# Kernel tuning notes

Hardware: AMD Instinct MI355X
Metric: run time of the kernel (lower is better)

Reference implementation:

```python
import jax, jax.numpy as jnp
import numpy as np
from itertools import combinations

UNSPOOL = np.array([h + b for h in combinations(range(0, 4), 2) for b in combinations(range(4, 9), 3)])  # (60,5)
EMB = 64

def _lrelu(v):
    return jax.nn.leaky_relu(v, 0.01)

def _unspool(x):
    # x: (M,18) int -> (1,M,60,5) ranks, suits
    x = x[None]
    ranks, suits = x[:, :, ::2], x[:, :, 1::2]
    hr, hs = ranks[:, :, :4], suits[:, :, :4]
    br, bs = ranks[:, :, 4:], suits[:, :, 4:]
    hi, bi = jnp.argsort(hs, -1), jnp.argsort(bs, -1)
    hr = jnp.take_along_axis(hr, hi, -1); hs = jnp.take_along_axis(hs, hi, -1)
    br = jnp.take_along_axis(br, bi, -1); bs = jnp.take_along_axis(bs, bi, -1)
    hi2, bi2 = jnp.argsort(hr, -1), jnp.argsort(br, -1)
    r = jnp.concatenate([jnp.take_along_axis(hr, hi2, -1), jnp.take_along_axis(br, bi2, -1)], -1)
    s = jnp.concatenate([jnp.take_along_axis(hs, hi2, -1), jnp.take_along_axis(bs, bi2, -1)], -1)
    return r[:, :, UNSPOOL], s[:, :, UNSPOOL]

def setup_inputs() -> dict:
    key = jax.random.key(0)
    ks = jax.random.split(key, 24)
    M, nA = 2048, 9
    ranks = jax.random.randint(ks[0], (M, 9), 1, 14)
    suits = jax.random.randint(ks[1], (M, 9), 1, 5)
    x = jnp.zeros((M, 18), jnp.int64 if jax.config.jax_enable_x64 else jnp.int32)
    x = x.at[:, ::2].set(ranks).at[:, 1::2].set(suits)
    def lin(k, i, o):
        kw, kb = jax.random.split(k)
        s = 1.0 / np.sqrt(i)
        return (jax.random.uniform(kw, (i, o), jnp.float32, -s, s),
                jax.random.uniform(kb, (o,), jnp.float32, -s, s))
    emb = jax.random.normal(ks[2], (53, EMB), jnp.float32)
    emb = emb.at[0].set(0.0)  # padding_idx=0
    hW1, hb1 = lin(ks[3], 128, 512); hW2, hb2 = lin(ks[4], 512, 128)
    bW1, bb1 = lin(ks[5], 192, 512); bW2, bb2 = lin(ks[6], 512, 128)
    oW1, ob1 = lin(ks[7], 15360, 512); oW2, ob2 = lin(ks[8], 512, 256); oW3, ob3 = lin(ks[9], 256, 127)
    sW, sb = lin(ks[10], 127, nA)
    return dict(x=x, emb=emb, hW1=hW1, hb1=hb1, hW2=hW2, hb2=hb2,
                bW1=bW1, bb1=bb1, bW2=bW2, bb2=bb2,
                oW1=oW1, ob1=ob1, oW2=oW2, ob2=ob2, oW3=oW3, ob3=ob3,
                sW=sW, sb=sb)

def reference(x, emb, hW1, hb1, hW2, hb2, bW1, bb1, bW2, bb2,
              oW1, ob1, oW2, ob2, oW3, ob3, sW, sb):
    M = x.shape[0]
    sr, ss = _unspool(x)                      # (1,M,60,5)
    cards = (sr - 1) * ss                     # 0..48, 0 is padding
    e = emb[cards]                            # (1,M,60,5,64)
    hero = e[..., :2, :].reshape(1, M, 60, 2 * EMB)    # (1,M,60,128)
    board = e[..., 2:, :].reshape(1, M, 60, 3 * EMB)   # (1,M,60,192)
    hero = _lrelu(_lrelu(hero @ hW1 + hb1) @ hW2 + hb2)
    board = _lrelu(_lrelu(board @ bW1 + bb1) @ bW2 + bb2)
    raw = jnp.concatenate([hero, board], -1).reshape(1, M, 60 * 256)  # (1,M,15360)
    r = _lrelu(raw @ oW1 + ob1)
    r = _lrelu(r @ oW2 + ob2)
    r = _lrelu(r @ oW3 + ob3)
    return r.reshape(M, -1) @ sW + sb         # (M,nA)
```

## Files before the change

### kernel.cpp

```cpp
#include <hip/hip_runtime.h>

typedef _Float16 f16;
typedef __attribute__((ext_vector_type(8))) _Float16 f16x8;
typedef __attribute__((ext_vector_type(4))) _Float16 f16x4;
typedef __attribute__((ext_vector_type(4))) float f32x4;
typedef __attribute__((ext_vector_type(16))) float f32x16;

__device__ inline float lrelu(float v){ return v > 0.f ? v : 0.01f*v; }
__device__ inline f16x8 lrelu8(f16x8 v){
    f16x8 z = {};
    f16x8 mx = __builtin_elementwise_max(v, z);
    f16x8 mn = __builtin_elementwise_min(v, z);
    return mx + mn * (f16)0.01f;
}

__device__ __forceinline__ void gload16(const void* gp, void* lp) {
    __builtin_amdgcn_global_load_lds(
        (const __attribute__((address_space(1))) unsigned int*)gp,
        (__attribute__((address_space(3))) unsigned int*)lp,
        16, 0, 0);
}

#define M_ROWS 2048

#define P1_T    0
#define P1_HW2  265
#define P1_BW2  393
#define P1_CARD 521
#define P1_END  525

__device__ void d_transpose512(const float* __restrict__ in, f16* __restrict__ out,
                               int K, int Nin, int Nout, int b, int tid) {
    int idx = b * 512 + tid;
    if (idx >= Nout * K) return;
    int n = idx / K, k = idx - n * K;
    float v = (n < Nin) ? in[(size_t)k * Nin + n] : 0.f;
    out[idx] = (f16)v;
}

__global__ __launch_bounds__(512) void prep1(const int* __restrict__ x,
                                             const float* __restrict__ emb,
                                             const float* __restrict__ hW1,
                                             const float* __restrict__ hb1,
                                             const float* __restrict__ hW2,
                                             const float* __restrict__ bW1,
                                             const float* __restrict__ bb1,
                                             const float* __restrict__ bW2,
                                             f16* __restrict__ T,
                                             f16* __restrict__ hW2t,
                                             f16* __restrict__ bW2t,
                                             int* __restrict__ cid) {
    const int bid = blockIdx.x, tid = threadIdx.x;
    if (bid < P1_HW2) {
        int b = bid;
        int slot = b / 53, card = b - slot * 53;
        const float* W = (slot < 2) ? (hW1 + slot * 64 * 512) : (bW1 + (slot - 2) * 64 * 512);
        const float* e = emb + card * 64;
        float acc = (slot == 1) ? hb1[tid] : ((slot == 4) ? bb1[tid] : 0.f);
        #pragma unroll 8
        for (int k = 0; k < 64; ++k) acc += e[k] * W[k * 512 + tid];
        T[(size_t)b * 512 + tid] = (f16)acc;
    } else if (bid < P1_BW2) {
        d_transpose512(hW2, hW2t, 512, 128, 128, bid - P1_HW2, tid);
    } else if (bid < P1_CARD) {
        d_transpose512(bW2, bW2t, 512, 128, 128, bid - P1_BW2, tid);
    } else {
        int m = (bid - P1_CARD) * 512 + tid;
        if (m >= M_ROWS) return;
        int kh[4], kb[5];
        #pragma unroll
        for (int i = 0; i < 4; ++i) { int r = x[m*18 + 2*i], s = x[m*18 + 2*i + 1]; kh[i] = r*8 + s; }
        #pragma unroll
        for (int i = 0; i < 5; ++i) { int r = x[m*18 + 8 + 2*i], s = x[m*18 + 9 + 2*i]; kb[i] = r*8 + s; }
        #pragma unroll
        for (int i = 1; i < 4; ++i) { int v = kh[i], j = i-1; while (j >= 0 && kh[j] > v) { kh[j+1]=kh[j]; --j; } kh[j+1]=v; }
        #pragma unroll
        for (int i = 1; i < 5; ++i) { int v = kb[i], j = i-1; while (j >= 0 && kb[j] > v) { kb[j+1]=kb[j]; --j; } kb[j+1]=v; }
        #pragma unroll
        for (int i = 0; i < 4; ++i) { int r = kh[i] >> 3, s = kh[i] & 7; cid[m*9 + i] = (r - 1) * s; }
        #pragma unroll
        for (int i = 0; i < 5; ++i) { int r = kb[i] >> 3, s = kb[i] & 7; cid[m*9 + 4 + i] = (r - 1) * s; }
    }
}

#define MG_L2   256
#define MG_OW2  768
#define MG_OW3  1024
#define MG_END  1088

__global__ __launch_bounds__(512, 4) void mega(const int* __restrict__ cid,
                                               const f16* __restrict__ T,
                                               const f16* __restrict__ hW2t,
                                               const f16* __restrict__ bW2t,
                                               const float* __restrict__ hb2,
                                               const float* __restrict__ bb2,
                                               const float* __restrict__ oW1,
                                               const float* __restrict__ oW2,
                                               const float* __restrict__ oW3,
                                               f16* __restrict__ X,
                                               f16* __restrict__ Wct,
                                               f16* __restrict__ oW2t,
                                               f16* __restrict__ oW3t) {
    __shared__ __align__(16) char smem[51200];
    const int bid = blockIdx.x, tid = threadIdx.x;

    if (bid < MG_L2) {
        float (*tile)[65] = (float(*)[65])smem;
        int kb = bid & 31, nb = bid >> 5;
        int nl = tid & 63;
        for (int kl = tid >> 6; kl < 64; kl += 8) {
            int col = kb * 64 + kl;
            int p = col >> 7, r = col & 127;
            int n = nb * 64 + nl;
            float s = 0.f;
            if (p < 6) {
                #pragma unroll
                for (int j = 0; j < 10; ++j) s += oW1[(size_t)((p * 10 + j) * 256 + r) * 512 + n];
            } else {
                int t = p - 6;
                #pragma unroll
                for (int i = 0; i < 6; ++i) s += oW1[(size_t)((i * 10 + t) * 256 + 128 + r) * 512 + n];
            }
            tile[kl][nl] = s;
        }
        __syncthreads();
        for (int nl2 = tid >> 6; nl2 < 64; nl2 += 8) {
            int kl2 = tid & 63;
            Wct[(size_t)(nb * 64 + nl2) * 2048 + kb * 64 + kl2] = (f16)tile[kl2][nl2];
        }
        return;
    }
    if (bid >= MG_OW3) {
        d_transpose512(oW3, oW3t, 256, 127, 128, bid - MG_OW3, tid);
        return;
    }
    if (bid >= MG_OW2) {
        d_transpose512(oW2, oW2t, 512, 256, 256, bid - MG_OW2, tid);
        return;
    }

    f16 (*As)[64*64]  = (f16(*)[64*64])smem;
    f16 (*Bs)[128*64] = (f16(*)[128*64])(smem + 16384);
    const int lbid = bid - MG_L2;
    const bool hero = lbid < 192;
    const int row0 = hero ? lbid * 64 : (lbid - 192) * 64;
    const f16* Bt = hero ? hW2t : bW2t;
    const float* bias = hero ? hb2 : bb2;
    const int lane = tid & 63, wave = tid >> 6;
    const int rw = wave & 1, cw = wave >> 1;
    const int l31 = lane & 31, lh = lane >> 5;

    const int br = tid >> 3, bchunk = tid & 7;
    const int grow = row0 + br;
    const f16 *t0, *t1, *t2;
    if (hero) {
        const int HP0[6] = {0,0,0,1,1,2}, HP1[6] = {1,2,3,2,3,3};
        int m = grow / 6, p = grow - m * 6;
        t0 = T + (size_t)(0*53 + cid[m*9 + HP0[p]]) * 512;
        t1 = T + (size_t)(1*53 + cid[m*9 + HP1[p]]) * 512;
        t2 = T;
    } else {
        const int BT0[10] = {4,4,4,4,4,4,5,5,5,6};
        const int BT1[10] = {5,5,5,6,6,7,6,6,7,7};
        const int BT2[10] = {6,7,8,7,8,8,7,8,8,8};
        int m = grow / 10, t = grow - m * 10;
        t0 = T + (size_t)(2*53 + cid[m*9 + BT0[t]]) * 512;
        t1 = T + (size_t)(3*53 + cid[m*9 + BT1[t]]) * 512;
        t2 = T + (size_t)(4*53 + cid[m*9 + BT2[t]]) * 512;
    }

    auto stageB = [&](int buf, int k0) {
        #pragma unroll
        for (int i = 0; i < 2; ++i) {
            int c = tid + i * 512;
            int r = c >> 3, cc = c & 7;
            gload16(Bt + (size_t)r * 512 + k0 + ((cc ^ (r & 7)) << 3), (void*)&Bs[buf][c * 8]);
        }
    };
    auto buildA = [&](int buf, int k0) {
        f16x8 a = *(const f16x8*)(t0 + k0 + bchunk * 8);
        f16x8 b = *(const f16x8*)(t1 + k0 + bchunk * 8);
        f16x8 c = *(const f16x8*)(t2 + k0 + bchunk * 8);
        *(f16x8*)&As[buf][br * 64 + ((bchunk ^ (br & 7)) << 3)] = lrelu8(a + b + c);
    };

    f32x16 acc = {};
    stageB(0, 0); buildA(0, 0);
    __syncthreads();
    for (int t = 0; t < 8; ++t) {
        int cur = t & 1;
        if (t < 7) { stageB(cur ^ 1, (t + 1) * 64); buildA(cur ^ 1, (t + 1) * 64); }
        #pragma unroll
        for (int ks4 = 0; ks4 < 4; ++ks4) {
            int chunk = ks4 * 2 + lh;
            int ar = rw * 32 + l31, bcol = cw * 32 + l31;
            f16x8 a = *(const f16x8*)&As[cur][ar * 64 + ((chunk ^ (ar & 7)) << 3)];
            f16x8 b = *(const f16x8*)&Bs[cur][bcol * 64 + ((chunk ^ (bcol & 7)) << 3)];
            acc = __builtin_amdgcn_mfma_f32_32x32x16_f16(a, b, acc, 0, 0, 0);
        }
        __syncthreads();
    }
    #pragma unroll
    for (int q = 0; q < 16; ++q) {
        int row = row0 + rw * 32 + (q & 3) + 8 * (q >> 2) + 4 * lh;
        int col = cw * 32 + l31;
        float v = lrelu(acc[q] + bias[col]);
        size_t off;
        if (hero) { int m = row / 6,  p = row - m*6;  off = (size_t)m*2048 + p*128 + col; }
        else      { int m = row / 10, p = row - m*10; off = (size_t)m*2048 + 768 + p*128 + col; }
        X[off] = (f16)v;
    }
}

__global__ __launch_bounds__(512, 4) void combine(const f16* __restrict__ X,
                                                  const f16* __restrict__ Wct,
                                                  float* __restrict__ R1p) {
    __shared__ __align__(16) f16 As[2][64 * 64];
    __shared__ __align__(16) f16 Bs[2][128 * 64];
    const int bid = blockIdx.x;
    const int xcd = bid & 7, slot = bid >> 3;
    const int rp = xcd * 4 + (slot & 3);
    const int rest = slot >> 2;
    const int cp = rest & 3, ks = rest >> 2;
    const int row0 = rp * 64, col0 = cp * 128, k0b = ks * 1024;
    const int tid = threadIdx.x, lane = tid & 63, wave = tid >> 6;
    const int rw = wave & 1, cw = wave >> 1;
    const int l31 = lane & 31, lh = lane >> 5;

    auto stage = [&](int buf, int k0) {
        { int r = tid >> 3, cc = tid & 7;
          gload16(X + (size_t)(row0 + r) * 2048 + k0 + ((cc ^ (r & 7)) << 3), (void*)&As[buf][tid * 8]); }
        #pragma unroll
        for (int i = 0; i < 2; ++i) {
            int c = tid + i * 512;
            int r = c >> 3, cc = c & 7;
            gload16(Wct + (size_t)(col0 + r) * 2048 + k0 + ((cc ^ (r & 7)) << 3), (void*)&Bs[buf][c * 8]);
        }
    };

    f32x16 acc = {};
    stage(0, k0b);
    __syncthreads();
    for (int t = 0; t < 16; ++t) {
        int cur = t & 1;
        if (t < 15) stage(cur ^ 1, k0b + (t + 1) * 64);
        #pragma unroll
        for (int ks4 = 0; ks4 < 4; ++ks4) {
            int chunk = ks4 * 2 + lh;
            int ar = rw * 32 + l31, bcol = cw * 32 + l31;
            f16x8 a = *(const f16x8*)&As[cur][ar * 64 + ((chunk ^ (ar & 7)) << 3)];
            f16x8 b = *(const f16x8*)&Bs[cur][bcol * 64 + ((chunk ^ (bcol & 7)) << 3)];
            acc = __builtin_amdgcn_mfma_f32_32x32x16_f16(a, b, acc, 0, 0, 0);
        }
        __syncthreads();
    }
    float* dst = R1p + (size_t)ks * 2048 * 512;
    #pragma unroll
    for (int q = 0; q < 16; ++q) {
        int row = row0 + rw * 32 + (q & 3) + 8 * (q >> 2) + 4 * lh;
        int col = col0 + cw * 32 + l31;
        dst[(size_t)row * 512 + col] = acc[q];
    }
}

__global__ __launch_bounds__(512, 2) void tail2(const float* __restrict__ R1p,
                                                const float* __restrict__ ob1,
                                                const f16* __restrict__ oW2t,
                                                const float* __restrict__ ob2,
                                                const f16* __restrict__ oW3t,
                                                const float* __restrict__ ob3,
                                                const float* __restrict__ sW,
                                                const float* __restrict__ sb,
                                                float* __restrict__ out) {
    __shared__ __align__(16) f16 A1s[16 * 512];
    __shared__ __align__(16) f16 Bs[2][256 * 64];
    __shared__ __align__(16) f16 R2s[16 * 256];
    __shared__ float R3s[16][132];
    __shared__ float sWs[127 * 9];
    __shared__ float sbs[9];
    const int row0 = blockIdx.x * 16;
    const int tid = threadIdx.x, lane = tid & 63, wave = tid >> 6;
    const int lr = lane & 15;

    auto stageB2 = [&](int buf, int t) {
        #pragma unroll
        for (int i = 0; i < 4; ++i) {
            int c = tid + i * 512;
            int r = c >> 3, cc = c & 7;
            gload16(oW2t + (size_t)r * 512 + t * 64 + ((cc ^ (r & 7)) << 3), (void*)&Bs[buf][c * 8]);
        }
    };
    stageB2(0, 0);

    #pragma unroll
    for (int i = 0; i < 4; ++i) {
        int g = tid + i * 512;
        int row = g >> 7, c4 = (g & 127) << 2;
        f32x4 a = *(const f32x4*)(R1p + (size_t)(row0 + row) * 512 + c4);
        f32x4 b = *(const f32x4*)(R1p + (size_t)2048 * 512 + (size_t)(row0 + row) * 512 + c4);
        f32x4 o = *(const f32x4*)(ob1 + c4);
        f16x4 p;
        #pragma unroll
        for (int q = 0; q < 4; ++q) p[q] = (f16)lrelu(a[q] + b[q] + o[q]);
        int chunk = c4 >> 3, half = (c4 >> 2) & 1;
        *(f16x4*)&A1s[row * 512 + ((chunk ^ (row & 7)) << 3) + half * 4] = p;
    }
    for (int i = tid; i < 127 * 9; i += 512) sWs[i] = sW[i];
    if (tid < 9) sbs[tid] = sb[tid];
    __syncthreads();

    f32x4 acc2[2] = {};
    for (int t = 0; t < 8; ++t) {
        int cur = t & 1;
        if (t < 7) stageB2(cur ^ 1, t + 1);
        #pragma unroll
        for (int kk2 = 0; kk2 < 2; ++kk2) {
            int g  = kk2 * 4 + (lane >> 4);
            int gg = t * 8 + g;
            f16x8 a = *(const f16x8*)&A1s[lr * 512 + ((gg ^ (lr & 7)) << 3)];
            int eo = (g ^ (lr & 7)) << 3;
            #pragma unroll
            for (int j = 0; j < 2; ++j) {
                f16x8 b = *(const f16x8*)&Bs[cur][(wave * 32 + j * 16 + lr) * 64 + eo];
                acc2[j] = __builtin_amdgcn_mfma_f32_16x16x32_f16(a, b, acc2[j], 0, 0, 0);
            }
        }
        __syncthreads();
    }
    #pragma unroll
    for (int j = 0; j < 2; ++j)
    #pragma unroll
    for (int q = 0; q < 4; ++q) {
        int row = (lane >> 4) * 4 + q;
        int col = wave * 32 + j * 16 + lr;
        f16 v = (f16)lrelu(acc2[j][q] + ob2[col]);
        int chunk = col >> 3, w = col & 7;
        R2s[row * 256 + ((chunk ^ (row & 7)) << 3) + w] = v;
    }
    auto stageB3 = [&](int buf, int t) {
        #pragma unroll
        for (int i = 0; i < 2; ++i) {
            int c = tid + i * 512;
            if (c < 1024) {
                int r = c >> 3, cc = c & 7;
                gload16(oW3t + (size_t)r * 256 + t * 64 + ((cc ^ (r & 7)) << 3), (void*)&Bs[buf][c * 8]);
            }
        }
    };
    stageB3(0, 0);
    __syncthreads();

    f32x4 acc3 = {};
    for (int t = 0; t < 4; ++t) {
        int cur = t & 1;
        if (t < 3) stageB3(cur ^ 1, t + 1);
        #pragma unroll
        for (int kk2 = 0; kk2 < 2; ++kk2) {
            int g  = kk2 * 4 + (lane >> 4);
            int gg = t * 8 + g;
            f16x8 a = *(const f16x8*)&R2s[lr * 256 + ((gg ^ (lr & 7)) << 3)];
            int eo = (g ^ (lr & 7)) << 3;
            f16x8 b = *(const f16x8*)&Bs[cur][(wave * 16 + lr) * 64 + eo];
            acc3 = __builtin_amdgcn_mfma_f32_16x16x32_f16(a, b, acc3, 0, 0, 0);
        }
        __syncthreads();
    }
    #pragma unroll
    for (int q = 0; q < 4; ++q) {
        int row = (lane >> 4) * 4 + q;
        int col = wave * 16 + lr;
        R3s[row][col] = lrelu(acc3[q] + ((col < 127) ? ob3[col] : 0.f));
    }
    __syncthreads();

    if (tid < 16 * 9) {
        int row = tid / 9, a = tid - row * 9;
        float s = sbs[a];
        #pragma unroll 4
        for (int n = 0; n < 127; ++n) s += R3s[row][n] * sWs[n * 9 + a];
        out[(size_t)(row0 + row) * 9 + a] = s;
    }
}

extern "C" void kernel_launch(void* const* d_in, const int* in_sizes, int n_in,
                              void* d_out, int out_size, void* d_ws, size_t ws_size,
                              hipStream_t stream) {
    const int*   x    = (const int*)  d_in[0];
    const float* emb  = (const float*)d_in[1];
    const float* hW1  = (const float*)d_in[2];
    const float* hb1  = (const float*)d_in[3];
    const float* hW2  = (const float*)d_in[4];
    const float* hb2  = (const float*)d_in[5];
    const float* bW1  = (const float*)d_in[6];
    const float* bb1  = (const float*)d_in[7];
    const float* bW2  = (const float*)d_in[8];
    const float* bb2  = (const float*)d_in[9];
    const float* oW1  = (const float*)d_in[10];
    const float* ob1  = (const float*)d_in[11];
    const float* oW2  = (const float*)d_in[12];
    const float* ob2  = (const float*)d_in[13];
    const float* oW3  = (const float*)d_in[14];
    const float* ob3  = (const float*)d_in[15];
    const float* sW   = (const float*)d_in[16];
    const float* sb   = (const float*)d_in[17];

    char* ws = (char*)d_ws;
    constexpr size_t OFF_T    = 0;
    constexpr size_t OFF_HW2T = 271360;
    constexpr size_t OFF_BW2T = 402432;
    constexpr size_t OFF_OW2T = 533504;
    constexpr size_t OFF_OW3T = 795648;
    constexpr size_t OFF_WCT  = 861184;
    constexpr size_t OFF_CID  = 2958336;
    constexpr size_t OFF_X    = 3032064;
    constexpr size_t OFF_R1P  = 11420672;

    f16*   T    = (f16*)(ws + OFF_T);
    f16*   hW2t = (f16*)(ws + OFF_HW2T);
    f16*   bW2t = (f16*)(ws + OFF_BW2T);
    f16*   oW2t = (f16*)(ws + OFF_OW2T);
    f16*   oW3t = (f16*)(ws + OFF_OW3T);
    f16*   Wct  = (f16*)(ws + OFF_WCT);
    int*   cid  = (int*)(ws + OFF_CID);
    f16*   X    = (f16*)(ws + OFF_X);
    float* R1p  = (float*)(ws + OFF_R1P);

    prep1<<<P1_END, 512, 0, stream>>>(x, emb, hW1, hb1, hW2, bW1, bb1, bW2,
                                      T, hW2t, bW2t, cid);
    mega<<<MG_END, 512, 0, stream>>>(cid, T, hW2t, bW2t, hb2, bb2,
                                     oW1, oW2, oW3, X, Wct, oW2t, oW3t);
    combine<<<256, 512, 0, stream>>>(X, Wct, R1p);
    tail2<<<128, 512, 0, stream>>>(R1p, ob1, oW2t, ob2, oW3t, ob3, sW, sb, (float*)d_out);
}
```

Before: 56.33 us.

## Split combine K four ways, halve tail rows per block, move transposes to prep1

The combine GEMM now splits K into four 512-wide slices over 512 blocks instead of two 1024-wide slices over 256 blocks, so more CUs get work. tail2 then sums four partial buffers and handles 8 rows per block over 256 blocks, zero-padding the unused half of its 16-row MFMA tile. The oW2/oW3 transposes move from mega into prep1, which shortens mega's grid. The cost is more partial-sum traffic through R1p, plus wasted MFMA work on the padded rows in tail2.

```diff
diff --git a/kernel.cpp b/kernel.cpp
--- a/kernel.cpp
+++ b/kernel.cpp
@@ -26,8 +26,10 @@
 #define P1_T    0
 #define P1_HW2  265
 #define P1_BW2  393
-#define P1_CARD 521
-#define P1_END  525
+#define P1_OW2  521
+#define P1_OW3  777
+#define P1_CARD 841
+#define P1_END  845
 
 __device__ void d_transpose512(const float* __restrict__ in, f16* __restrict__ out,
                                int K, int Nin, int Nout, int b, int tid) {
@@ -46,9 +48,13 @@
                                              const float* __restrict__ bW1,
                                              const float* __restrict__ bb1,
                                              const float* __restrict__ bW2,
+                                             const float* __restrict__ oW2,
+                                             const float* __restrict__ oW3,
                                              f16* __restrict__ T,
                                              f16* __restrict__ hW2t,
                                              f16* __restrict__ bW2t,
+                                             f16* __restrict__ oW2t,
+                                             f16* __restrict__ oW3t,
                                              int* __restrict__ cid) {
     const int bid = blockIdx.x, tid = threadIdx.x;
     if (bid < P1_HW2) {
@@ -62,8 +68,12 @@
         T[(size_t)b * 512 + tid] = (f16)acc;
     } else if (bid < P1_BW2) {
         d_transpose512(hW2, hW2t, 512, 128, 128, bid - P1_HW2, tid);
+    } else if (bid < P1_OW2) {
+        d_transpose512(bW2, bW2t, 512, 128, 128, bid - P1_BW2, tid);
+    } else if (bid < P1_OW3) {
+        d_transpose512(oW2, oW2t, 512, 256, 256, bid - P1_OW2, tid);
     } else if (bid < P1_CARD) {
-        d_transpose512(bW2, bW2t, 512, 128, 128, bid - P1_BW2, tid);
+        d_transpose512(oW3, oW3t, 256, 127, 128, bid - P1_OW3, tid);
     } else {
         int m = (bid - P1_CARD) * 512 + tid;
         if (m >= M_ROWS) return;
@@ -84,9 +94,7 @@
 }
 
 #define MG_L2   256
-#define MG_OW2  768
-#define MG_OW3  1024
-#define MG_END  1088
+#define MG_END  768
 
 __global__ __launch_bounds__(512, 4) void mega(const int* __restrict__ cid,
                                                const f16* __restrict__ T,
@@ -95,12 +103,8 @@
                                                const float* __restrict__ hb2,
                                                const float* __restrict__ bb2,
                                                const float* __restrict__ oW1,
-                                               const float* __restrict__ oW2,
-                                               const float* __restrict__ oW3,
                                                f16* __restrict__ X,
-                                               f16* __restrict__ Wct,
-                                               f16* __restrict__ oW2t,
-                                               f16* __restrict__ oW3t) {
+                                               f16* __restrict__ Wct) {
     __shared__ __align__(16) char smem[51200];
     const int bid = blockIdx.x, tid = threadIdx.x;
 
@@ -130,14 +134,6 @@
         }
         return;
     }
-    if (bid >= MG_OW3) {
-        d_transpose512(oW3, oW3t, 256, 127, 128, bid - MG_OW3, tid);
-        return;
-    }
-    if (bid >= MG_OW2) {
-        d_transpose512(oW2, oW2t, 512, 256, 256, bid - MG_OW2, tid);
-        return;
-    }
 
     f16 (*As)[64*64]  = (f16(*)[64*64])smem;
     f16 (*Bs)[128*64] = (f16(*)[128*64])(smem + 16384);
@@ -222,7 +218,7 @@
     const int rp = xcd * 4 + (slot & 3);
     const int rest = slot >> 2;
     const int cp = rest & 3, ks = rest >> 2;
-    const int row0 = rp * 64, col0 = cp * 128, k0b = ks * 1024;
+    const int row0 = rp * 64, col0 = cp * 128, k0b = ks * 512;
     const int tid = threadIdx.x, lane = tid & 63, wave = tid >> 6;
     const int rw = wave & 1, cw = wave >> 1;
     const int l31 = lane & 31, lh = lane >> 5;
@@ -241,9 +237,9 @@
     f32x16 acc = {};
     stage(0, k0b);
     __syncthreads();
-    for (int t = 0; t < 16; ++t) {
+    for (int t = 0; t < 8; ++t) {
         int cur = t & 1;
-        if (t < 15) stage(cur ^ 1, k0b + (t + 1) * 64);
+        if (t < 7) stage(cur ^ 1, k0b + (t + 1) * 64);
         #pragma unroll
         for (int ks4 = 0; ks4 < 4; ++ks4) {
             int chunk = ks4 * 2 + lh;
@@ -278,7 +274,7 @@
     __shared__ float R3s[16][132];
     __shared__ float sWs[127 * 9];
     __shared__ float sbs[9];
-    const int row0 = blockIdx.x * 16;
+    const int row0 = blockIdx.x * 8;
     const int tid = threadIdx.x, lane = tid & 63, wave = tid >> 6;
     const int lr = lane & 15;
 
@@ -293,17 +289,23 @@
     stageB2(0, 0);
 
     #pragma unroll
-    for (int i = 0; i < 4; ++i) {
+    for (int i = 0; i < 2; ++i) {
         int g = tid + i * 512;
         int row = g >> 7, c4 = (g & 127) << 2;
-        f32x4 a = *(const f32x4*)(R1p + (size_t)(row0 + row) * 512 + c4);
-        f32x4 b = *(const f32x4*)(R1p + (size_t)2048 * 512 + (size_t)(row0 + row) * 512 + c4);
-        f32x4 o = *(const f32x4*)(ob1 + c4);
+        f32x4 v = *(const f32x4*)(ob1 + c4);
+        #pragma unroll
+        for (int s = 0; s < 4; ++s)
+            v += *(const f32x4*)(R1p + (size_t)s * 2048 * 512 + (size_t)(row0 + row) * 512 + c4);
         f16x4 p;
         #pragma unroll
-        for (int q = 0; q < 4; ++q) p[q] = (f16)lrelu(a[q] + b[q] + o[q]);
+        for (int q = 0; q < 4; ++q) p[q] = (f16)lrelu(v[q]);
         int chunk = c4 >> 3, half = (c4 >> 2) & 1;
         *(f16x4*)&A1s[row * 512 + ((chunk ^ (row & 7)) << 3) + half * 4] = p;
+    }
+    {
+        f16x8 z = {};
+        int row = 8 + (tid >> 6), chunk = tid & 63;
+        *(f16x8*)&A1s[row * 512 + chunk * 8] = z;
     }
     for (int i = tid; i < 127 * 9; i += 512) sWs[i] = sW[i];
     if (tid < 9) sbs[tid] = sb[tid];
@@ -373,7 +375,7 @@
     }
     __syncthreads();
 
-    if (tid < 16 * 9) {
+    if (tid < 8 * 9) {
         int row = tid / 9, a = tid - row * 9;
         float s = sbs[a];
         #pragma unroll 4
@@ -426,9 +428,8 @@
     float* R1p  = (float*)(ws + OFF_R1P);
 
     prep1<<<P1_END, 512, 0, stream>>>(x, emb, hW1, hb1, hW2, bW1, bb1, bW2,
-                                      T, hW2t, bW2t, cid);
-    mega<<<MG_END, 512, 0, stream>>>(cid, T, hW2t, bW2t, hb2, bb2,
-                                     oW1, oW2, oW3, X, Wct, oW2t, oW3t);
-    combine<<<256, 512, 0, stream>>>(X, Wct, R1p);
-    tail2<<<128, 512, 0, stream>>>(R1p, ob1, oW2t, ob2, oW3t, ob3, sW, sb, (float*)d_out);
-}
+                                      oW2, oW3, T, hW2t, bW2t, oW2t, oW3t, cid);
+    mega<<<MG_END, 512, 0, stream>>>(cid, T, hW2t, bW2t, hb2, bb2, oW1, X, Wct);
+    combine<<<512, 512, 0, stream>>>(X, Wct, R1p);
+    tail2<<<256, 512, 0, stream>>>(R1p, ob1, oW2t, ob2, oW3t, ob3, sW, sb, (float*)d_out);
+}
```

Result: faster. 53.68 us (median of 2 runs) (-4.7%).
